# Kernel optimization log

Hardware: AMD Instinct MI355X
Metric: run time of the kernel (lower is better)

Reference implementation:

```python
import jax, jax.numpy as jnp
import numpy as np

NUM_GROUPS = 32
EPS = 1e-6


def group_norm(x, gamma, beta):
    # x: [B, C, H, W]; GroupNorm over (channels-in-group, H, W)
    B, C, H, W = x.shape
    xg = x.reshape(B, NUM_GROUPS, C // NUM_GROUPS, H, W)
    mean = xg.mean(axis=(2, 3, 4), keepdims=True)
    var = xg.var(axis=(2, 3, 4), keepdims=True)
    xn = ((xg - mean) * jax.lax.rsqrt(var + EPS)).reshape(B, C, H, W)
    return xn * gamma[None, :, None, None] + beta[None, :, None, None]


def conv1x1(x, w, b):
    # 1x1 conv == channel-mixing matmul. w: [C_out, C_in]
    return jnp.einsum('bchw,oc->bohw', x, w) + b[None, :, None, None]


def setup_inputs() -> dict:
    key = jax.random.key(0)
    ks = jax.random.split(key, 6)
    B, C, H, W = 8, 256, 64, 64
    s = 1.0 / np.sqrt(C)  # fan-in scaled weights (like Conv2d default)
    inp = {
        'x': jax.random.normal(ks[0], (B, C, H, W), jnp.float32),
        'gamma': jnp.ones((C,), jnp.float32),
        'beta': jnp.zeros((C,), jnp.float32),
        'wq': jax.random.normal(ks[1], (C, C), jnp.float32) * s,
        'bq': jnp.zeros((C,), jnp.float32),
        'wk': jax.random.normal(ks[2], (C, C), jnp.float32) * s,
        'bk': jnp.zeros((C,), jnp.float32),
        'wv': jax.random.normal(ks[3], (C, C), jnp.float32) * s,
        'bv': jnp.zeros((C,), jnp.float32),
        'wo': jax.random.normal(ks[4], (C, C), jnp.float32) * s,
        'bo': jnp.zeros((C,), jnp.float32),
    }
    return inp


def reference(x, gamma, beta, wq, bq, wk, bk, wv, bv, wo, bo):
    B, C, H, W = x.shape
    h = group_norm(x, gamma, beta)
    q = conv1x1(h, wq, bq)
    k = conv1x1(h, wk, bk)
    v = conv1x1(h, wv, bv)
    # elu + 1 feature map (nonnegative kernel features)
    q = jax.nn.elu(q) + 1.0
    k = jax.nn.elu(k) + 1.0
    N = H * W
    kf = k.reshape(B, C, N)            # [B, C, N]
    vf = v.reshape(B, C, N)            # [B, C, N]
    qf = q.reshape(B, C, N)            # [B, C, N]
    # kv = k @ v^T : [B, C, C]
    kv = jnp.einsum('bcn,bdn->bcd', kf, vf)
    # h_out[b, n, d] = sum_c q[b, c, n] * kv[b, c, d]; stored channel-first
    h_out = jnp.einsum('bcn,bcd->bdn', qf, kv).reshape(B, C, H, W)
    return x + conv1x1(h_out, wo, bo)
```

## Files before the change

### kernel.cpp

```cpp
#include <hip/hip_runtime.h>
#include <math.h>

#define C_DIM 256
#define N_DIM 4096
#define B_DIM 8

typedef __attribute__((ext_vector_type(8))) short bf16x8;
typedef __attribute__((ext_vector_type(4))) float f32x4;
typedef __attribute__((ext_vector_type(8))) unsigned short us8;
typedef __attribute__((ext_vector_type(4))) unsigned short us4;

__device__ inline unsigned short f2bf(float f) {
    unsigned int u = __float_as_uint(f);
    u += 0x7fffu + ((u >> 16) & 1u);
    return (unsigned short)(u >> 16);
}

__device__ inline void gload_lds16(const void* g, void* l) {
    __builtin_amdgcn_global_load_lds(
        (const __attribute__((address_space(1))) unsigned int*)g,
        (__attribute__((address_space(3))) unsigned int*)l, 16, 0, 0);
}

__global__ __launch_bounds__(256) void transx(const float* __restrict__ x,
                                              unsigned short* __restrict__ xT,
                                              float2* __restrict__ pst) {
    int b = blockIdx.y, nt = blockIdx.x, n0 = nt * 64;
    int t = threadIdx.x;
    __shared__ unsigned short trans[64][264];

    #pragma unroll
    for (int it = 0; it < 16; it++) {
        int c  = it*16 + (t >> 4);
        int nl = (t & 15) * 4;
        float4 v = *(const float4*)(x + ((size_t)(b*C_DIM + c))*N_DIM + n0 + nl);
        trans[nl+0][c] = f2bf(v.x);
        trans[nl+1][c] = f2bf(v.y);
        trans[nl+2][c] = f2bf(v.z);
        trans[nl+3][c] = f2bf(v.w);
        float s4 = v.x + v.y + v.z + v.w;
        float q4 = v.x*v.x + v.y*v.y + v.z*v.z + v.w*v.w;
        #pragma unroll
        for (int m = 1; m < 16; m <<= 1) {
            s4 += __shfl_xor(s4, m);
            q4 += __shfl_xor(q4, m);
        }
        if ((t & 15) == 0)
            pst[(size_t)(b*64 + nt)*256 + c] = make_float2(s4, q4);
    }
    __syncthreads();

    #pragma unroll
    for (int it = 0; it < 8; it++) {
        int nl = it*8 + (t >> 5);
        int cb = (t & 31) * 8;
        us8 vv = *(us8*)&trans[nl][cb];
        *(us8*)(xT + ((size_t)b*N_DIM + n0 + nl)*C_DIM + cb) = vv;
    }
}

__global__ __launch_bounds__(256) void fold(
    const float* __restrict__ wq, const float* __restrict__ wk,
    const float* __restrict__ wv, const float* __restrict__ wo,
    const float* __restrict__ bq, const float* __restrict__ bk,
    const float* __restrict__ bv,
    const float* __restrict__ gamma, const float* __restrict__ beta,
    const float2* __restrict__ pst,
    unsigned short* __restrict__ wqb2, unsigned short* __restrict__ wkvb2,
    unsigned short* __restrict__ wob,
    float* __restrict__ bq2, float* __restrict__ bkv2)
{
    int z = blockIdx.y;
    int t = threadIdx.x;
    if (z == 12) {
        int base = blockIdx.x * 8192;
        #pragma unroll
        for (int i = 0; i < 8; i++) {
            int idx = base + i*1024 + t*4;
            float4 v = *(const float4*)(wo + idx);
            us4 r; r[0]=f2bf(v.x); r[1]=f2bf(v.y); r[2]=f2bf(v.z); r[3]=f2bf(v.w);
            *(us4*)(wob + idx) = r;
        }
        return;
    }
    int b = blockIdx.x;
    __shared__ float scale[256], shift[256], chS[256], chQ[256];

    float S = 0.f, Q = 0.f;
    for (int nt = 0; nt < 64; nt++) {
        float2 u = pst[(size_t)(b*64 + nt)*256 + t];
        S += u.x; Q += u.y;
    }
    chS[t] = S; chQ[t] = Q;
    __syncthreads();
    {
        int gb = t & ~7;
        float Sg = 0.f, Qg = 0.f;
        #pragma unroll
        for (int j = 0; j < 8; j++) { Sg += chS[gb+j]; Qg += chQ[gb+j]; }
        float mean = Sg * (1.f/32768.f);
        float var  = Qg * (1.f/32768.f) - mean*mean;
        float inv  = rsqrtf(var + 1e-6f);
        float sc = gamma[t] * inv;
        scale[t] = sc;
        shift[t] = beta[t] - mean * sc;
    }
    __syncthreads();

    int r0 = z * 64;
    const float* Wsrc; const float* bsrc; unsigned short* dst; float* bdst;
    if (r0 < 256)      { int r=r0;     Wsrc=wq+(size_t)r*256; bsrc=bq+r; dst=wqb2 +(size_t)b*65536 +(size_t)r*256;      bdst=bq2 +b*256+r; }
    else if (r0 < 512) { int r=r0-256; Wsrc=wk+(size_t)r*256; bsrc=bk+r; dst=wkvb2+(size_t)b*131072+(size_t)r*256;      bdst=bkv2+b*512+r; }
    else               { int r=r0-512; Wsrc=wv+(size_t)r*256; bsrc=bv+r; dst=wkvb2+(size_t)b*131072+(size_t)(r+256)*256; bdst=bkv2+b*512+256+r; }

    #pragma unroll
    for (int i = 0; i < 16; i++) {
        int idx = t + 256*i;
        int row = idx >> 6, c4 = (idx & 63) * 4;
        float4 v = *(const float4*)(Wsrc + (size_t)row*256 + c4);
        us4 r;
        r[0] = f2bf(v.x * scale[c4+0]);
        r[1] = f2bf(v.y * scale[c4+1]);
        r[2] = f2bf(v.z * scale[c4+2]);
        r[3] = f2bf(v.w * scale[c4+3]);
        *(us4*)(dst + (size_t)row*256 + c4) = r;
    }

    {
        int row = t >> 2, qd = t & 3;
        float p = 0.f;
        for (int i = 0; i < 64; i++) {
            int c = qd*64 + i;
            p += Wsrc[(size_t)row*256 + c] * shift[c];
        }
        chS[t] = p;
        __syncthreads();
        if (t < 64)
            bdst[t] = bsrc[t] + chS[t*4] + chS[t*4+1] + chS[t*4+2] + chS[t*4+3];
    }
}

template<int MODE>
__device__ __forceinline__ void gemm_body(
    const unsigned short* __restrict__ Ab, const unsigned short* __restrict__ Bb,
    const float* __restrict__ bias, const float* __restrict__ residb,
    void* __restrict__ Cb,
    int N, int K, int k0, int Ks, int m_blk, int n_blk, bool elu,
    char* smem)
{
    unsigned short* As0 = (unsigned short*)smem;
    unsigned short* Bs0 = As0 + 4096;
    unsigned short* As1 = As0 + 8192;
    unsigned short* Bs1 = As0 + 12288;

    int t = threadIdx.x;
    int w = t >> 6, l = t & 63;
    int wm = w >> 1, wn = w & 1;
    int l15 = l & 15, quad = l >> 4;

    int srow = w * 16 + (l >> 2);
    int skc  = (l & 3) * 8;

    f32x4 acc[4][4];
    #pragma unroll
    for (int i = 0; i < 4; i++)
        #pragma unroll
        for (int j = 0; j < 4; j++)
            #pragma unroll
            for (int r = 0; r < 4; r++) acc[i][j][r] = 0.f;

    int fro = (wm*64 + l15)*32 + quad*8;
    int fco = (wn*64 + l15)*32 + quad*8;
    int sl  = w*512 + l*8;

    for (int kt = k0; kt < k0 + Ks; kt += 64) {
        #pragma unroll
        for (int rep = 0; rep < 2; rep++) {
            size_t ga = (size_t)(m_blk + rep*64 + srow) * K + kt + skc;
            size_t gb = (size_t)(n_blk + rep*64 + srow) * K + kt + skc;
            gload_lds16(Ab + ga,      As0 + sl + rep*2048);
            gload_lds16(Bb + gb,      Bs0 + sl + rep*2048);
            gload_lds16(Ab + ga + 32, As1 + sl + rep*2048);
            gload_lds16(Bb + gb + 32, Bs1 + sl + rep*2048);
        }
        __syncthreads();
        {
            bf16x8 af[4], bfr[4];
            #pragma unroll
            for (int i = 0; i < 4; i++) af[i]  = *(const bf16x8*)(As0 + fro + i*512);
            #pragma unroll
            for (int j = 0; j < 4; j++) bfr[j] = *(const bf16x8*)(Bs0 + fco + j*512);
            #pragma unroll
            for (int i = 0; i < 4; i++)
                #pragma unroll
                for (int j = 0; j < 4; j++)
                    acc[i][j] = __builtin_amdgcn_mfma_f32_16x16x32_bf16(af[i], bfr[j], acc[i][j], 0, 0, 0);
            #pragma unroll
            for (int i = 0; i < 4; i++) af[i]  = *(const bf16x8*)(As1 + fro + i*512);
            #pragma unroll
            for (int j = 0; j < 4; j++) bfr[j] = *(const bf16x8*)(Bs1 + fco + j*512);
            #pragma unroll
            for (int i = 0; i < 4; i++)
                #pragma unroll
                for (int j = 0; j < 4; j++)
                    acc[i][j] = __builtin_amdgcn_mfma_f32_16x16x32_bf16(af[i], bfr[j], acc[i][j], 0, 0, 0);
        }
        __syncthreads();
    }

    if (MODE == 0 || MODE == 1) {
        unsigned short* ep = (unsigned short*)smem;
        int row0 = wm*64 + quad*4;
        int col0 = wn*64 + l15;
        #pragma unroll
        for (int i = 0; i < 4; i++) {
            #pragma unroll
            for (int j = 0; j < 4; j++) {
                int cl = col0 + j*16;
                #pragma unroll
                for (int r = 0; r < 4; r++) {
                    int rl = row0 + i*16 + r;
                    float val = acc[i][j][r];
                    if (MODE == 0) {
                        val += bias[n_blk + cl];
                        val = val > 0.f ? val + 1.f : __expf(val);
                    } else {
                        val += bias[m_blk + rl];
                        if (elu) val = val > 0.f ? val + 1.f : __expf(val);
                    }
                    ep[rl*136 + cl] = f2bf(val);
                }
            }
        }
        __syncthreads();
        unsigned short* Cp = (unsigned short*)Cb;
        #pragma unroll
        for (int it = 0; it < 8; it++) {
            int row = it*16 + (t >> 4);
            int col = (t & 15) * 8;
            us8 vv = *(us8*)(ep + row*136 + col);
            *(us8*)(Cp + (size_t)(m_blk + row) * N + n_blk + col) = vv;
        }
    } else {
        float* ep32 = (float*)smem;
        float* Cp = (float*)Cb;
        #pragma unroll
        for (int h = 0; h < 2; h++) {
            if (wm == h) {
                int row0 = quad*4;
                int col0 = wn*64 + l15;
                #pragma unroll
                for (int i = 0; i < 4; i++)
                    #pragma unroll
                    for (int j = 0; j < 4; j++)
                        #pragma unroll
                        for (int r = 0; r < 4; r++)
                            ep32[(row0 + i*16 + r)*140 + col0 + j*16] = acc[i][j][r];
            }
            __syncthreads();
            #pragma unroll
            for (int it = 0; it < 8; it++) {
                int rl  = it*8 + (t >> 5);
                int row = m_blk + h*64 + rl;
                int col = (t & 31) * 4;
                f32x4 vv = *(f32x4*)(ep32 + rl*140 + col);
                if (MODE == 5) {
                    float bi = bias[row];
                    float4 rv = *(const float4*)(residb + (size_t)row * N + n_blk + col);
                    vv[0] += bi + rv.x; vv[1] += bi + rv.y;
                    vv[2] += bi + rv.z; vv[3] += bi + rv.w;
                }
                *(f32x4*)(Cp + (size_t)row * N + n_blk + col) = vv;
            }
            __syncthreads();
        }
    }
}

__global__ __launch_bounds__(256) void qkv_kernel(
    const unsigned short* __restrict__ xT,
    const unsigned short* __restrict__ wqb2, const unsigned short* __restrict__ wkvb2,
    const float* __restrict__ bq2, const float* __restrict__ bkv2,
    unsigned short* __restrict__ qT, unsigned short* __restrict__ kvbuf)
{
    __shared__ __align__(16) char smem[36864];
    int z = blockIdx.x;
    if (z < 512) {
        int b = z >> 6, rem = z & 63;
        int m_blk = (rem >> 1) * 128, n_blk = (rem & 1) * 128;
        gemm_body<0>(xT + (size_t)b*1048576, wqb2 + (size_t)b*65536,
                     bq2 + b*256, nullptr,
                     qT + (size_t)b*1048576,
                     256, 256, 0, 256, m_blk, n_blk, true, smem);
    } else {
        int iz = z - 512;
        int b = iz >> 7, rem = iz & 127;
        int m_blk = (rem >> 5) * 128, n_blk = (rem & 31) * 128;
        gemm_body<1>(wkvb2 + (size_t)b*131072, xT + (size_t)b*1048576,
                     bkv2 + b*512, nullptr,
                     kvbuf + (size_t)b*2097152,
                     4096, 256, 0, 256, m_blk, n_blk, m_blk < 256, smem);
    }
}

__global__ __launch_bounds__(256) void kv_kernel(const unsigned short* __restrict__ kvbuf,
                                                 float* __restrict__ kvf)
{
    __shared__ __align__(16) char smem[36864];
    int b = blockIdx.z >> 4, sp = blockIdx.z & 15;
    gemm_body<3>(kvbuf + (size_t)b*2097152, kvbuf + (size_t)b*2097152 + 1048576,
                 nullptr, nullptr,
                 kvf + (size_t)(b*16 + sp)*65536,
                 256, 4096, sp*256, 256, blockIdx.y*128, blockIdx.x*128, false, smem);
}

__global__ __launch_bounds__(256) void m2red(const float* __restrict__ kvf,
                                             const unsigned short* __restrict__ wob,
                                             unsigned short* __restrict__ M2b)
{
    __shared__ __align__(16) unsigned short smem2[67584];
    unsigned short* Bsf = smem2;
    unsigned short* Asf = smem2 + 33792;

    int b = blockIdx.z, m_blk = blockIdx.y*128, n_blk = blockIdx.x*128;
    int t = threadIdx.x;

    #pragma unroll
    for (int i = 0; i < 32; i++) {
        int j = t + 256*i;
        int c = j >> 6, c4 = (j & 63) * 4;
        float4 a = make_float4(0.f,0.f,0.f,0.f);
        #pragma unroll
        for (int sp = 0; sp < 16; sp++) {
            float4 v = *(const float4*)(kvf + ((size_t)(b*16+sp) << 16) + (size_t)(n_blk + c)*256 + c4);
            a.x += v.x; a.y += v.y; a.z += v.z; a.w += v.w;
        }
        us4 r; r[0]=f2bf(a.x); r[1]=f2bf(a.y); r[2]=f2bf(a.z); r[3]=f2bf(a.w);
        *(us4*)(Bsf + c*264 + c4) = r;
    }
    #pragma unroll
    for (int i = 0; i < 16; i++) {
        int j = t + 256*i;
        int row = j >> 5, col8 = (j & 31) * 8;
        us8 v = *(const us8*)(wob + (size_t)(m_blk + row)*256 + col8);
        *(us8*)(Asf + row*264 + col8) = v;
    }
    __syncthreads();

    int w = t >> 6, l = t & 63;
    int wm = w >> 1, wn = w & 1;
    int l15 = l & 15, quad = l >> 4;

    f32x4 acc[4][4];
    #pragma unroll
    for (int i = 0; i < 4; i++)
        #pragma unroll
        for (int j = 0; j < 4; j++)
            #pragma unroll
            for (int r = 0; r < 4; r++) acc[i][j][r] = 0.f;

    #pragma unroll
    for (int kc = 0; kc < 8; kc++) {
        bf16x8 af[4], bfr[4];
        #pragma unroll
        for (int i = 0; i < 4; i++)
            af[i]  = *(const bf16x8*)(Asf + (wm*64 + i*16 + l15)*264 + kc*32 + quad*8);
        #pragma unroll
        for (int j = 0; j < 4; j++)
            bfr[j] = *(const bf16x8*)(Bsf + (wn*64 + j*16 + l15)*264 + kc*32 + quad*8);
        #pragma unroll
        for (int i = 0; i < 4; i++)
            #pragma unroll
            for (int j = 0; j < 4; j++)
                acc[i][j] = __builtin_amdgcn_mfma_f32_16x16x32_bf16(af[i], bfr[j], acc[i][j], 0, 0, 0);
    }
    __syncthreads();

    unsigned short* ep = Asf;
    int row0 = wm*64 + quad*4;
    int col0 = wn*64 + l15;
    #pragma unroll
    for (int i = 0; i < 4; i++)
        #pragma unroll
        for (int j = 0; j < 4; j++)
            #pragma unroll
            for (int r = 0; r < 4; r++)
                ep[(row0 + i*16 + r)*136 + col0 + j*16] = f2bf(acc[i][j][r]);
    __syncthreads();
    #pragma unroll
    for (int it = 0; it < 8; it++) {
        int row = it*16 + (t >> 4);
        int col = (t & 15) * 8;
        us8 vv = *(us8*)(ep + row*136 + col);
        *(us8*)(M2b + (size_t)b*65536 + (size_t)(m_blk + row)*256 + n_blk + col) = vv;
    }
}

__global__ __launch_bounds__(256) void out_kernel(const unsigned short* __restrict__ M2b,
                                                  const unsigned short* __restrict__ qT,
                                                  const float* __restrict__ bo,
                                                  const float* __restrict__ x,
                                                  float* __restrict__ outp)
{
    __shared__ __align__(16) char smem[36864];
    int b = blockIdx.z;
    gemm_body<5>(M2b + (size_t)b*65536, qT + (size_t)b*1048576,
                 bo, x + (size_t)b*1048576,
                 outp + (size_t)b*1048576,
                 4096, 256, 0, 256, blockIdx.y*128, blockIdx.x*128, false, smem);
}

extern "C" void kernel_launch(void* const* d_in, const int* in_sizes, int n_in,
                              void* d_out, int out_size, void* d_ws, size_t ws_size,
                              hipStream_t stream) {
    const float* x     = (const float*)d_in[0];
    const float* gamma = (const float*)d_in[1];
    const float* beta  = (const float*)d_in[2];
    const float* wq    = (const float*)d_in[3];
    const float* bq    = (const float*)d_in[4];
    const float* wk    = (const float*)d_in[5];
    const float* bk    = (const float*)d_in[6];
    const float* wv    = (const float*)d_in[7];
    const float* bv    = (const float*)d_in[8];
    const float* wo    = (const float*)d_in[9];
    const float* bo    = (const float*)d_in[10];
    float* out = (float*)d_out;

    const size_t TEN = (size_t)B_DIM * C_DIM * N_DIM;
    unsigned short* ws16  = (unsigned short*)d_ws;
    unsigned short* xT    = ws16;
    unsigned short* qT    = xT    + TEN;
    unsigned short* kvbuf = qT    + TEN;
    unsigned short* wqb2  = kvbuf + 2*TEN;
    unsigned short* wkvb2 = wqb2  + 524288;
    unsigned short* wob   = wkvb2 + 1048576;
    unsigned short* M2b   = wob   + 65536;
    float*          bq2   = (float*)(M2b + 524288);
    float*          bkv2  = bq2   + 2048;
    float2*         pst   = (float2*)(bkv2 + 4096);
    float*          kvf   = (float*)(pst + 131072);

    transx<<<dim3(64, B_DIM), 256, 0, stream>>>(x, xT, pst);
    fold<<<dim3(8, 13), 256, 0, stream>>>(wq, wk, wv, wo, bq, bk, bv, gamma, beta,
                                          pst, wqb2, wkvb2, wob, bq2, bkv2);
    qkv_kernel<<<dim3(1536), 256, 0, stream>>>(xT, wqb2, wkvb2, bq2, bkv2, qT, kvbuf);
    kv_kernel<<<dim3(2, 2, B_DIM*16), 256, 0, stream>>>(kvbuf, kvf);
    m2red<<<dim3(2, 2, B_DIM), 256, 0, stream>>>(kvf, wob, M2b);
    out_kernel<<<dim3(32, 2, B_DIM), 256, 0, stream>>>(M2b, qT, bo, x, out);
}
```

Measured before the change: 213.4 us.

## Split split-K reduction into separate kernel and reuse generic GEMM for M2

The fused m2red kernel, which summed 16 split-K partials of kv and then multiplied by Wo in one 32-block grid, is replaced by two kernels. A 512-block elementwise reduction kernel converts the summed kv to bf16, and m2_kernel then runs the shared pipelined gemm_body (MODE 4) on it. The aim is to spread the memory-bound partial-sum reduction over many more blocks instead of 32 large-LDS blocks. The cost is an extra kernel launch and a bf16 round trip through global memory.

```diff
diff --git a/kernel.cpp b/kernel.cpp
--- a/kernel.cpp
+++ b/kernel.cpp
@@ -140,6 +140,19 @@
     }
 }
 
+__global__ __launch_bounds__(256) void kvred(const float* __restrict__ src, unsigned short* __restrict__ dst) {
+    int gi = (blockIdx.x * 256 + threadIdx.x) * 4;
+    int b = gi >> 16, idx = gi & 65535;
+    float4 a = make_float4(0.f,0.f,0.f,0.f);
+    #pragma unroll
+    for (int sp = 0; sp < 16; sp++) {
+        float4 v = *(const float4*)(src + (((size_t)b*16 + sp) << 16) + idx);
+        a.x += v.x; a.y += v.y; a.z += v.z; a.w += v.w;
+    }
+    us4 r; r[0] = f2bf(a.x); r[1] = f2bf(a.y); r[2] = f2bf(a.z); r[3] = f2bf(a.w);
+    *(us4*)(dst + ((size_t)b << 16) + idx) = r;
+}
+
 template<int MODE>
 __device__ __forceinline__ void gemm_body(
     const unsigned short* __restrict__ Ab, const unsigned short* __restrict__ Bb,
@@ -208,7 +221,7 @@
         __syncthreads();
     }
 
-    if (MODE == 0 || MODE == 1) {
+    if (MODE == 0 || MODE == 1 || MODE == 4) {
         unsigned short* ep = (unsigned short*)smem;
         int row0 = wm*64 + quad*4;
         int col0 = wn*64 + l15;
@@ -224,7 +237,7 @@
                     if (MODE == 0) {
                         val += bias[n_blk + cl];
                         val = val > 0.f ? val + 1.f : __expf(val);
-                    } else {
+                    } else if (MODE == 1) {
                         val += bias[m_blk + rl];
                         if (elu) val = val > 0.f ? val + 1.f : __expf(val);
                     }
@@ -314,86 +327,16 @@
                  256, 4096, sp*256, 256, blockIdx.y*128, blockIdx.x*128, false, smem);
 }
 
-__global__ __launch_bounds__(256) void m2red(const float* __restrict__ kvf,
-                                             const unsigned short* __restrict__ wob,
-                                             unsigned short* __restrict__ M2b)
-{
-    __shared__ __align__(16) unsigned short smem2[67584];
-    unsigned short* Bsf = smem2;
-    unsigned short* Asf = smem2 + 33792;
-
-    int b = blockIdx.z, m_blk = blockIdx.y*128, n_blk = blockIdx.x*128;
-    int t = threadIdx.x;
-
-    #pragma unroll
-    for (int i = 0; i < 32; i++) {
-        int j = t + 256*i;
-        int c = j >> 6, c4 = (j & 63) * 4;
-        float4 a = make_float4(0.f,0.f,0.f,0.f);
-        #pragma unroll
-        for (int sp = 0; sp < 16; sp++) {
-            float4 v = *(const float4*)(kvf + ((size_t)(b*16+sp) << 16) + (size_t)(n_blk + c)*256 + c4);
-            a.x += v.x; a.y += v.y; a.z += v.z; a.w += v.w;
-        }
-        us4 r; r[0]=f2bf(a.x); r[1]=f2bf(a.y); r[2]=f2bf(a.z); r[3]=f2bf(a.w);
-        *(us4*)(Bsf + c*264 + c4) = r;
-    }
-    #pragma unroll
-    for (int i = 0; i < 16; i++) {
-        int j = t + 256*i;
-        int row = j >> 5, col8 = (j & 31) * 8;
-        us8 v = *(const us8*)(wob + (size_t)(m_blk + row)*256 + col8);
-        *(us8*)(Asf + row*264 + col8) = v;
-    }
-    __syncthreads();
-
-    int w = t >> 6, l = t & 63;
-    int wm = w >> 1, wn = w & 1;
-    int l15 = l & 15, quad = l >> 4;
-
-    f32x4 acc[4][4];
-    #pragma unroll
-    for (int i = 0; i < 4; i++)
-        #pragma unroll
-        for (int j = 0; j < 4; j++)
-            #pragma unroll
-            for (int r = 0; r < 4; r++) acc[i][j][r] = 0.f;
-
-    #pragma unroll
-    for (int kc = 0; kc < 8; kc++) {
-        bf16x8 af[4], bfr[4];
-        #pragma unroll
-        for (int i = 0; i < 4; i++)
-            af[i]  = *(const bf16x8*)(Asf + (wm*64 + i*16 + l15)*264 + kc*32 + quad*8);
-        #pragma unroll
-        for (int j = 0; j < 4; j++)
-            bfr[j] = *(const bf16x8*)(Bsf + (wn*64 + j*16 + l15)*264 + kc*32 + quad*8);
-        #pragma unroll
-        for (int i = 0; i < 4; i++)
-            #pragma unroll
-            for (int j = 0; j < 4; j++)
-                acc[i][j] = __builtin_amdgcn_mfma_f32_16x16x32_bf16(af[i], bfr[j], acc[i][j], 0, 0, 0);
-    }
-    __syncthreads();
-
-    unsigned short* ep = Asf;
-    int row0 = wm*64 + quad*4;
-    int col0 = wn*64 + l15;
-    #pragma unroll
-    for (int i = 0; i < 4; i++)
-        #pragma unroll
-        for (int j = 0; j < 4; j++)
-            #pragma unroll
-            for (int r = 0; r < 4; r++)
-                ep[(row0 + i*16 + r)*136 + col0 + j*16] = f2bf(acc[i][j][r]);
-    __syncthreads();
-    #pragma unroll
-    for (int it = 0; it < 8; it++) {
-        int row = it*16 + (t >> 4);
-        int col = (t & 15) * 8;
-        us8 vv = *(us8*)(ep + row*136 + col);
-        *(us8*)(M2b + (size_t)b*65536 + (size_t)(m_blk + row)*256 + n_blk + col) = vv;
-    }
+__global__ __launch_bounds__(256) void m2_kernel(const unsigned short* __restrict__ wob,
+                                                 const unsigned short* __restrict__ kvb,
+                                                 unsigned short* __restrict__ M2b)
+{
+    __shared__ __align__(16) char smem[36864];
+    int b = blockIdx.z;
+    gemm_body<4>(wob, kvb + (size_t)b*65536,
+                 nullptr, nullptr,
+                 M2b + (size_t)b*65536,
+                 256, 256, 0, 256, blockIdx.y*128, blockIdx.x*128, false, smem);
 }
 
 __global__ __launch_bounds__(256) void out_kernel(const unsigned short* __restrict__ M2b,
@@ -435,7 +378,8 @@
     unsigned short* wkvb2 = wqb2  + 524288;
     unsigned short* wob   = wkvb2 + 1048576;
     unsigned short* M2b   = wob   + 65536;
-    float*          bq2   = (float*)(M2b + 524288);
+    unsigned short* kvb   = M2b   + 524288;
+    float*          bq2   = (float*)(kvb + 524288);
     float*          bkv2  = bq2   + 2048;
     float2*         pst   = (float2*)(bkv2 + 4096);
     float*          kvf   = (float*)(pst + 131072);
@@ -445,6 +389,7 @@
                                           pst, wqb2, wkvb2, wob, bq2, bkv2);
     qkv_kernel<<<dim3(1536), 256, 0, stream>>>(xT, wqb2, wkvb2, bq2, bkv2, qT, kvbuf);
     kv_kernel<<<dim3(2, 2, B_DIM*16), 256, 0, stream>>>(kvbuf, kvf);
-    m2red<<<dim3(2, 2, B_DIM), 256, 0, stream>>>(kvf, wob, M2b);
+    kvred<<<dim3(512), 256, 0, stream>>>(kvf, kvb);
+    m2_kernel<<<dim3(2, 2, B_DIM), 256, 0, stream>>>(wob, kvb, M2b);
     out_kernel<<<dim3(32, 2, B_DIM), 256, 0, stream>>>(M2b, qT, bo, x, out);
 }
```

Result: faster. 187.7 us (-12.1%).
